# Kernel tuning notes

Measured on AMD Instinct MI355X. Metric: run time of the kernel, lower is better.

Reference implementation:

```python
import math
import jax, jax.numpy as jnp
import numpy as np

N_EMBD = 1024
N_HEAD = 16
HEAD_DIM = N_EMBD // N_HEAD
B, T = 4, 2048
LN_EPS = 1e-5


def setup_inputs() -> dict:
    key = jax.random.key(0)
    ks = jax.random.split(key, 20)
    s = 0.02
    d = {
        'x': jax.random.normal(ks[0], (B, T, N_EMBD), jnp.float32),
        'Wq': jax.random.normal(ks[1], (N_EMBD, N_EMBD), jnp.float32) * s,
        'bq': jnp.zeros((N_EMBD,), jnp.float32),
        'Wk': jax.random.normal(ks[2], (N_EMBD, N_EMBD), jnp.float32) * s,
        'bk': jnp.zeros((N_EMBD,), jnp.float32),
        'Wv': jax.random.normal(ks[3], (N_EMBD, N_EMBD), jnp.float32) * s,
        'bv': jnp.zeros((N_EMBD,), jnp.float32),
        'Wo': jax.random.normal(ks[4], (N_EMBD, N_EMBD), jnp.float32) * s,
        'bo': jnp.zeros((N_EMBD,), jnp.float32),
        'ln1_g': jnp.ones((N_EMBD,), jnp.float32),
        'ln1_b': jnp.zeros((N_EMBD,), jnp.float32),
        'ln2_g': jnp.ones((N_EMBD,), jnp.float32),
        'ln2_b': jnp.zeros((N_EMBD,), jnp.float32),
        'W_fc': jax.random.normal(ks[5], (N_EMBD, 4 * N_EMBD), jnp.float32) * s,
        'b_fc': jnp.zeros((4 * N_EMBD,), jnp.float32),
        'W_proj': jax.random.normal(ks[6], (4 * N_EMBD, N_EMBD), jnp.float32) * s,
        'b_proj': jnp.zeros((N_EMBD,), jnp.float32),
    }
    return d


def _layernorm(x, g, b):
    mu = jnp.mean(x, axis=-1, keepdims=True)
    var = jnp.var(x, axis=-1, keepdims=True)
    return (x - mu) * jax.lax.rsqrt(var + LN_EPS) * g + b


def _new_gelu(x):
    c = math.sqrt(2.0 / math.pi)
    return 0.5 * x * (1.0 + jnp.tanh(c * (x + 0.044715 * x ** 3)))


def _attn(x, Wq, bq, Wk, bk, Wv, bv, Wo, bo):
    Bq, Tq, C = x.shape
    def heads(y):  # (B,T,C) -> (B,H,T,D)
        return y.reshape(Bq, Tq, N_HEAD, HEAD_DIM).transpose(0, 2, 1, 3)
    q = heads(x @ Wq + bq)
    k = heads(x @ Wk + bk)
    v = heads(x @ Wv + bv)
    scores = jnp.einsum('bhqd,bhkd->bhqk', q, k) / math.sqrt(HEAD_DIM)
    causal = jnp.tril(jnp.ones((Tq, Tq), bool))
    scores = jnp.where(causal, scores, -jnp.inf)
    w = jax.nn.softmax(scores, axis=-1)
    av = jnp.einsum('bhqk,bhkd->bhqd', w, v)
    av = av.transpose(0, 2, 1, 3).reshape(Bq, Tq, C)
    return av @ Wo + bo


def reference(x, Wq, bq, Wk, bk, Wv, bv, Wo, bo, ln1_g, ln1_b, ln2_g, ln2_b, W_fc, b_fc, W_proj, b_proj):
    x = x + _attn(_layernorm(x, ln1_g, ln1_b), Wq, bq, Wk, bk, Wv, bv, Wo, bo)
    h = _layernorm(x, ln2_g, ln2_b)
    x = x + (_new_gelu(h @ W_fc + b_fc) @ W_proj + b_proj)
    return x
```

## Files before the change

### kernel.cpp

```cpp
#include <hip/hip_runtime.h>

typedef __attribute__((ext_vector_type(8))) short short8;
typedef __attribute__((ext_vector_type(4))) short short4v;
typedef __attribute__((ext_vector_type(4))) float floatx4;
typedef unsigned short u16;

#define MFMA16(a,b,c) __builtin_amdgcn_mfma_f32_16x16x32_bf16(a,b,c,0,0,0)

typedef const __attribute__((address_space(1))) void* gas1;
typedef __attribute__((address_space(3))) void* las3;
static __device__ __forceinline__ void glds16(const void* g, void* l){
  __builtin_amdgcn_global_load_lds((gas1)g, (las3)l, 16, 0, 0);
}

static __device__ __forceinline__ u16 f2b(float f){
  union { float f; unsigned int u; } c; c.f = f;
  unsigned int u = c.u;
  u += 0x7fffu + ((u >> 16) & 1u);
  return (u16)(u >> 16);
}

__global__ __launch_bounds__(256) void transpose_cvt(
    const float* __restrict__ W, u16* __restrict__ Wt, int K, int N){
  __shared__ float tile[32][33];
  const int tx = threadIdx.x & 31;
  const int ty = threadIdx.x >> 5;
  const int nx = blockIdx.x * 32, kx = blockIdx.y * 32;
  #pragma unroll
  for (int i = ty; i < 32; i += 8)
    tile[i][tx] = W[(size_t)(kx + i) * N + nx + tx];
  __syncthreads();
  #pragma unroll
  for (int i = ty; i < 32; i += 8)
    Wt[(size_t)(nx + i) * K + kx + tx] = f2b(tile[tx][i]);
}

__global__ __launch_bounds__(256) void ln_kernel(
    const float* __restrict__ x, const float* __restrict__ g,
    const float* __restrict__ b, u16* __restrict__ out){
  const int row = blockIdx.x, tid = threadIdx.x;
  const float4 v = reinterpret_cast<const float4*>(x + (size_t)row * 1024)[tid];
  float s  = v.x + v.y + v.z + v.w;
  float s2 = v.x*v.x + v.y*v.y + v.z*v.z + v.w*v.w;
  #pragma unroll
  for (int off = 1; off < 64; off <<= 1){
    s  += __shfl_xor(s,  off);
    s2 += __shfl_xor(s2, off);
  }
  __shared__ float red[8];
  const int wave = tid >> 6, lane = tid & 63;
  if (lane == 0){ red[wave] = s; red[4 + wave] = s2; }
  __syncthreads();
  s  = red[0] + red[1] + red[2] + red[3];
  s2 = red[4] + red[5] + red[6] + red[7];
  const float mu  = s * (1.f/1024.f);
  const float var = s2 * (1.f/1024.f) - mu * mu;
  const float rs  = rsqrtf(var + 1e-5f);
  const float4 gg = reinterpret_cast<const float4*>(g)[tid];
  const float4 bb = reinterpret_cast<const float4*>(b)[tid];
  ushort4 o;
  o.x = f2b((v.x - mu) * rs * gg.x + bb.x);
  o.y = f2b((v.y - mu) * rs * gg.y + bb.y);
  o.z = f2b((v.z - mu) * rs * gg.z + bb.z);
  o.w = f2b((v.w - mu) * rs * gg.w + bb.w);
  reinterpret_cast<ushort4*>(out + (size_t)row * 1024)[tid] = o;
}

__global__ __launch_bounds__(256) void bias_concat(
    const float* __restrict__ bq, const float* __restrict__ bk,
    const float* __restrict__ bv, float* __restrict__ o){
  const int i = blockIdx.x * 256 + threadIdx.x;
  if (i < 1024) o[i] = bq[i];
  else if (i < 2048) o[i] = bk[i - 1024];
  else if (i < 3072) o[i] = bv[i - 2048];
}

template<bool GELU, bool RES, bool OUTBF, bool QKVMODE>
__global__ __launch_bounds__(512) void gemm256(
    const u16* __restrict__ A, const u16* __restrict__ Bt,
    const float* __restrict__ bias,
    const float* __restrict__ res,
    float* __restrict__ outF, u16* __restrict__ outB,
    u16* __restrict__ vtb,
    int M, int N, int K)
{
  __shared__ __attribute__((aligned(16))) u16 sA[2][2][256 * 32];
  __shared__ __attribute__((aligned(16))) u16 sB[2][2][256 * 32];
  const int tid  = threadIdx.x;
  const int wave = tid >> 6, lane = tid & 63, ql = lane >> 4, l16 = lane & 15;
  const int wr = wave >> 2, wc = wave & 3;
  const int m0 = blockIdx.x * 256, n0 = blockIdx.y * 256;

  const int scol = ((lane & 3) ^ ((lane >> 3) & 3)) * 8;
  const u16* aBase = A  + (size_t)(m0 + wave*16 + (lane >> 2)) * K + scol;
  const u16* bBase = Bt + (size_t)(n0 + wr*64 + 4*(lane >> 2) + wc) * K + scol;
  const size_t hK = (size_t)128 * K;
  const int qx = (ql ^ ((l16 >> 1) & 3)) * 8;

  floatx4 acc[8][4];
  #pragma unroll
  for (int i = 0; i < 8; i++)
    #pragma unroll
    for (int nt = 0; nt < 4; nt++) acc[i][nt] = floatx4{0.f,0.f,0.f,0.f};
  short8 af[4], bf[4];

#define STAGE(B_, T_) do { \
    const size_t ko_ = (size_t)(T_) * 64; \
    glds16(aBase + ko_,           &sA[B_][0][wave*512]); \
    glds16(aBase + ko_ + 32,      &sA[B_][1][wave*512]); \
    glds16(aBase + ko_ + hK,      &sA[B_][0][4096 + wave*512]); \
    glds16(aBase + ko_ + hK + 32, &sA[B_][1][4096 + wave*512]); \
    glds16(bBase + ko_,           &sB[B_][0][wave*512]); \
    glds16(bBase + ko_ + 32,      &sB[B_][1][wave*512]); \
    glds16(bBase + ko_ + hK,      &sB[B_][0][4096 + wave*512]); \
    glds16(bBase + ko_ + hK + 32, &sB[B_][1][4096 + wave*512]); \
  } while(0)
#define LDA(B_, KH_, Q_) do { \
    _Pragma("unroll") \
    for (int ii_ = 0; ii_ < 4; ii_++) \
      af[ii_] = *reinterpret_cast<const short8*>( \
          &sA[B_][KH_][(wr*128 + (Q_)*64 + ii_*16 + l16)*32 + qx]); \
  } while(0)
#define LDB(B_, KH_) do { \
    _Pragma("unroll") \
    for (int nt_ = 0; nt_ < 4; nt_++) \
      bf[nt_] = *reinterpret_cast<const short8*>( \
          &sB[B_][KH_][(wc*64 + nt_*16 + l16)*32 + qx]); \
  } while(0)
#define MM(Q_) do { \
    __builtin_amdgcn_s_setprio(1); \
    _Pragma("unroll") \
    for (int ii_ = 0; ii_ < 4; ii_++) \
      _Pragma("unroll") \
      for (int nt_ = 0; nt_ < 4; nt_++) \
        acc[(Q_)*4 + ii_][nt_] = MFMA16(af[ii_], bf[nt_], acc[(Q_)*4 + ii_][nt_]); \
    __builtin_amdgcn_s_setprio(0); \
  } while(0)
#define BAR() do { asm volatile("" ::: "memory"); \
    __builtin_amdgcn_s_barrier(); asm volatile("" ::: "memory"); } while(0)
#define WAITV(N_) asm volatile("s_waitcnt vmcnt(" #N_ ")" ::: "memory")

  const int ntile = K >> 6;
  STAGE(0, 0);

  #pragma unroll 1
  for (int t = 0; t < ntile; t += 2){
    STAGE(1, t + 1);
    WAITV(8);
    BAR();
    LDB(0, 0); LDA(0, 0, 0); MM(0);
    BAR();
    LDA(0, 0, 1); BAR(); MM(1); BAR();
    LDB(0, 1); LDA(0, 1, 0); BAR(); MM(0); BAR();
    LDA(0, 1, 1); BAR(); MM(1); BAR();
    if (t + 2 < ntile){ STAGE(0, t + 2); WAITV(8); }
    else              { WAITV(0); }
    BAR();
    LDB(1, 0); LDA(1, 0, 0); MM(0);
    BAR();
    LDA(1, 0, 1); BAR(); MM(1); BAR();
    LDB(1, 1); LDA(1, 1, 0); BAR(); MM(0); BAR();
    LDA(1, 1, 1); BAR(); MM(1); BAR();
  }

#undef STAGE
#undef LDA
#undef LDB
#undef MM
#undef BAR
#undef WAITV

  const int col0 = n0 + wc*64 + 4*l16;
  const floatx4 bi = *reinterpret_cast<const floatx4*>(&bias[col0]);

  if (QKVMODE && n0 >= 2048){
    #pragma unroll
    for (int nt = 0; nt < 4; nt++){
      const int hd = col0 + nt - 2048;
      u16* vcol = vtb + (size_t)(hd >> 6) * 131072 + (size_t)(hd & 63) * 2048;
      #pragma unroll
      for (int i = 0; i < 8; i++){
        const int t0 = m0 + wr*128 + i*16 + ql*4;
        const int bb = t0 >> 11, tt = t0 & 2047;
        short4v pk;
        #pragma unroll
        for (int r = 0; r < 4; r++) pk[r] = (short)f2b(acc[i][nt][r] + bi[nt]);
        *reinterpret_cast<short4v*>(vcol + (size_t)bb * 2097152 + tt) = pk;
      }
    }
    return;
  }

  #pragma unroll
  for (int i = 0; i < 8; i++){
    #pragma unroll
    for (int r = 0; r < 4; r++){
      const int row = m0 + wr*128 + i*16 + ql*4 + r;
      if (OUTBF){
        short4v o;
        #pragma unroll
        for (int nt = 0; nt < 4; nt++){
          float val = acc[i][nt][r] + bi[nt];
          if (GELU){
            const float t = 0.7978845608028654f * (val + 0.044715f * val * val * val);
            val = val / (1.f + __expf(-2.f * t));
          }
          o[nt] = (short)f2b(val);
        }
        *reinterpret_cast<short4v*>(&outB[(size_t)row * N + col0]) = o;
      } else {
        floatx4 v;
        #pragma unroll
        for (int nt = 0; nt < 4; nt++) v[nt] = acc[i][nt][r] + bi[nt];
        if (RES){
          const floatx4 rr = *reinterpret_cast<const floatx4*>(&res[(size_t)row * N + col0]);
          #pragma unroll
          for (int nt = 0; nt < 4; nt++) v[nt] += rr[nt];
        }
        *reinterpret_cast<floatx4*>(&outF[(size_t)row * N + col0]) = v;
      }
    }
  }
}

__global__ __launch_bounds__(256) void attn_kernel(
    const u16* __restrict__ qkv, const u16* __restrict__ vtb,
    u16* __restrict__ O)
{
  constexpr int T = 2048, LDQ = 3072, LDP = 72;
  __shared__ __attribute__((aligned(16))) u16 sK[2][2][64*32];
  __shared__ __attribute__((aligned(16))) u16 sV[2][2][64*32];
  __shared__ __attribute__((aligned(16))) u16 sP[4][16*LDP];

  const int tid = threadIdx.x, wave = tid >> 6, lane = tid & 63;
  const int quad = lane >> 4, l16 = lane & 15;

  const int lin = blockIdx.y * 16 + blockIdx.x;
  const int j = lin & 15;
  const int bh = lin >> 4;
  const int kk4 = bh >> 4;
  const int jj = (j + ((kk4 & 2) << 2)) & 15;
  const int qt = (kk4 & 1) ? (15 - jj) : jj;
  const int q0 = qt * 128;
  const int b = bh >> 4, h = bh & 15;

  const u16* Qp = qkv + (size_t)b * T * LDQ + h * 64;
  const u16* Kp = Qp + 1024;
  const u16* Vt = vtb + (size_t)bh * 64 * T;

  const int qx = (quad ^ ((l16 >> 1) & 3)) * 8;

  int qg[2]; qg[0] = q0 + wave*16 + l16; qg[1] = qg[0] + 64;
  short8 qf[2][2];
  #pragma unroll
  for (int g = 0; g < 2; g++){
    qf[g][0] = *reinterpret_cast<const short8*>(&Qp[(size_t)qg[g]*LDQ + quad*8]);
    qf[g][1] = *reinterpret_cast<const short8*>(&Qp[(size_t)qg[g]*LDQ + 32 + quad*8]);
  }

  float m_i[2] = {-INFINITY, -INFINITY}, l_i[2] = {0.f, 0.f};
  floatx4 o_acc[2][4];
  #pragma unroll
  for (int g = 0; g < 2; g++)
    #pragma unroll
    for (int nt = 0; nt < 4; nt++) o_acc[g][nt] = floatx4{0.f,0.f,0.f,0.f};

  const int srow = wave*16 + (lane >> 2);
  const int scol = ((lane & 3) ^ ((lane >> 3) & 3)) * 8;
  const int asrc = (lane & 48) | (quad * 4);

  const int kend = q0 + 128;

  {
    glds16(Kp + (size_t)srow*LDQ + scol,      sK[0][0] + wave*512);
    glds16(Kp + (size_t)srow*LDQ + 32 + scol, sK[0][1] + wave*512);
    glds16(Vt + (size_t)srow*T + scol,        sV[0][0] + wave*512);
    glds16(Vt + (size_t)srow*T + 32 + scol,   sV[0][1] + wave*512);
  }

  int buf = 0;
  for (int k0 = 0; k0 < kend; k0 += 64, buf ^= 1){
    __syncthreads();
    if (k0 + 64 < kend){
      const int kn = k0 + 64;
      glds16(Kp + (size_t)(kn + srow)*LDQ + scol,      sK[buf^1][0] + wave*512);
      glds16(Kp + (size_t)(kn + srow)*LDQ + 32 + scol, sK[buf^1][1] + wave*512);
      glds16(Vt + (size_t)srow*T + kn + scol,          sV[buf^1][0] + wave*512);
      glds16(Vt + (size_t)srow*T + kn + 32 + scol,     sV[buf^1][1] + wave*512);
    }

    #pragma unroll
    for (int g = 0; g < 2; g++){
      if (g == 0 && k0 > q0) continue;

      float s[4][4];
      #pragma unroll
      for (int sub = 0; sub < 4; sub++){
        floatx4 sa = floatx4{0.f,0.f,0.f,0.f};
        const short8 kf0 = *reinterpret_cast<const short8*>(&sK[buf][0][(sub*16 + l16)*32 + qx]);
        const short8 kf1 = *reinterpret_cast<const short8*>(&sK[buf][1][(sub*16 + l16)*32 + qx]);
        sa = MFMA16(kf0, qf[g][0], sa);
        sa = MFMA16(kf1, qf[g][1], sa);
        #pragma unroll
        for (int r = 0; r < 4; r++) s[sub][r] = sa[r];
      }
      if (k0 == q0 + g*64){
        #pragma unroll
        for (int sub = 0; sub < 4; sub++)
          #pragma unroll
          for (int r = 0; r < 4; r++){
            const int kidx = k0 + sub*16 + quad*4 + r;
            if (kidx > qg[g]) s[sub][r] = -1e30f;
          }
      }

      float mx = s[0][0];
      #pragma unroll
      for (int sub = 0; sub < 4; sub++)
        #pragma unroll
        for (int r = 0; r < 4; r++) mx = fmaxf(mx, s[sub][r]);
      mx = fmaxf(mx, __shfl_xor(mx, 16));
      mx = fmaxf(mx, __shfl_xor(mx, 32));
      const float mnew  = fmaxf(m_i[g], mx);
      const float alpha = __expf(0.125f * (m_i[g] - mnew));
      float p[4][4], rowsum = 0.f;
      #pragma unroll
      for (int sub = 0; sub < 4; sub++)
        #pragma unroll
        for (int r = 0; r < 4; r++){
          p[sub][r] = __expf(0.125f * (s[sub][r] - mnew));
          rowsum += p[sub][r];
        }
      rowsum += __shfl_xor(rowsum, 16);
      rowsum += __shfl_xor(rowsum, 32);
      l_i[g] = l_i[g] * alpha + rowsum;
      m_i[g] = mnew;

      float arow[4];
      #pragma unroll
      for (int r = 0; r < 4; r++) arow[r] = __shfl(alpha, asrc + r);
      #pragma unroll
      for (int nt = 0; nt < 4; nt++)
        #pragma unroll
        for (int r = 0; r < 4; r++) o_acc[g][nt][r] *= arow[r];

      #pragma unroll
      for (int sub = 0; sub < 4; sub++){
        short4v pk;
        pk[0] = (short)f2b(p[sub][0]); pk[1] = (short)f2b(p[sub][1]);
        pk[2] = (short)f2b(p[sub][2]); pk[3] = (short)f2b(p[sub][3]);
        *reinterpret_cast<short4v*>(&sP[wave][l16*LDP + sub*16 + quad*4]) = pk;
      }
      const short8 pf0 = *reinterpret_cast<const short8*>(&sP[wave][l16*LDP + quad*8]);
      const short8 pf1 = *reinterpret_cast<const short8*>(&sP[wave][l16*LDP + 32 + quad*8]);
      #pragma unroll
      for (int nt = 0; nt < 4; nt++){
        const short8 vf0 = *reinterpret_cast<const short8*>(&sV[buf][0][(nt*16 + l16)*32 + qx]);
        const short8 vf1 = *reinterpret_cast<const short8*>(&sV[buf][1][(nt*16 + l16)*32 + qx]);
        o_acc[g][nt] = MFMA16(pf0, vf0, o_acc[g][nt]);
        o_acc[g][nt] = MFMA16(pf1, vf1, o_acc[g][nt]);
      }
    }
  }

  #pragma unroll
  for (int g = 0; g < 2; g++){
    float lrow[4];
    #pragma unroll
    for (int r = 0; r < 4; r++) lrow[r] = __shfl(l_i[g], asrc + r);
    #pragma unroll
    for (int nt = 0; nt < 4; nt++){
      #pragma unroll
      for (int r = 0; r < 4; r++){
        const int row = q0 + g*64 + wave*16 + quad*4 + r;
        O[(size_t)(b*T + row)*1024 + h*64 + nt*16 + l16] = f2b(o_acc[g][nt][r] / lrow[r]);
      }
    }
  }
}

extern "C" void kernel_launch(void* const* d_in, const int* in_sizes, int n_in,
                              void* d_out, int out_size, void* d_ws, size_t ws_size,
                              hipStream_t stream){
  const float* x      = (const float*)d_in[0];
  const float* Wq     = (const float*)d_in[1];
  const float* bq     = (const float*)d_in[2];
  const float* Wk     = (const float*)d_in[3];
  const float* bk     = (const float*)d_in[4];
  const float* Wv     = (const float*)d_in[5];
  const float* bv     = (const float*)d_in[6];
  const float* Wo     = (const float*)d_in[7];
  const float* bo     = (const float*)d_in[8];
  const float* ln1_g  = (const float*)d_in[9];
  const float* ln1_b  = (const float*)d_in[10];
  const float* ln2_g  = (const float*)d_in[11];
  const float* ln2_b  = (const float*)d_in[12];
  const float* W_fc   = (const float*)d_in[13];
  const float* b_fc   = (const float*)d_in[14];
  const float* W_proj = (const float*)d_in[15];
  const float* b_proj = (const float*)d_in[16];
  float* out = (float*)d_out;
  char* ws = (char*)d_ws;
  const size_t MB = 1024 * 1024;

  u16* bufA  = (u16*)(ws);
  u16* qkvb  = (u16*)(ws + 16*MB);
  u16* vtb   = (u16*)(ws + 64*MB);
  u16* fcb   = (u16*)(ws + 16*MB);
  float* x2  = out;
  u16* Wqkvt = (u16*)(ws + 80*MB);
  u16* Wot   = (u16*)(ws + 86*MB);
  u16* Wfct  = (u16*)(ws + 88*MB);
  u16* Wpjt  = (u16*)(ws + 96*MB);
  float* bqkv= (float*)(ws + 104*MB);

  dim3 tb(256), tg(512);
  transpose_cvt<<<dim3(32, 32),  tb, 0, stream>>>(Wq,     Wqkvt,             1024, 1024);
  transpose_cvt<<<dim3(32, 32),  tb, 0, stream>>>(Wk,     Wqkvt + 1024*1024, 1024, 1024);
  transpose_cvt<<<dim3(32, 32),  tb, 0, stream>>>(Wv,     Wqkvt + 2048*1024, 1024, 1024);
  transpose_cvt<<<dim3(32, 32),  tb, 0, stream>>>(Wo,     Wot,               1024, 1024);
  transpose_cvt<<<dim3(128, 32), tb, 0, stream>>>(W_fc,   Wfct,              1024, 4096);
  transpose_cvt<<<dim3(32, 128), tb, 0, stream>>>(W_proj, Wpjt,              4096, 1024);
  bias_concat<<<dim3(12), tb, 0, stream>>>(bq, bk, bv, bqkv);

  ln_kernel<<<8192, tb, 0, stream>>>(x, ln1_g, ln1_b, bufA);

  gemm256<false,false,true,true><<<dim3(32,12), tg, 0, stream>>>(
      bufA, Wqkvt, bqkv, nullptr, nullptr, qkvb, vtb, 8192, 3072, 1024);

  attn_kernel<<<dim3(16, 64), tb, 0, stream>>>(qkvb, vtb, bufA);

  gemm256<false,true,false,false><<<dim3(32,4), tg, 0, stream>>>(
      bufA, Wot, bo, x, x2, nullptr, nullptr, 8192, 1024, 1024);

  ln_kernel<<<8192, tb, 0, stream>>>(x2, ln2_g, ln2_b, bufA);

  gemm256<true,false,true,false><<<dim3(32,16), tg, 0, stream>>>(
      bufA, Wfct, b_fc, nullptr, nullptr, fcb, nullptr, 8192, 4096, 1024);

  gemm256<false,true,false,false><<<dim3(32,4), tg, 0, stream>>>(
      fcb, Wpjt, b_proj, x2, out, nullptr, nullptr, 8192, 1024, 4096);
}
```

Measured before the change: 616.3 us.

## Interleave global-to-LDS prefetch in quarters between MFMA phases of GEMM mainloop

Splits each K-tile's global-to-LDS stage into four partial loads (A and B halves by K-subtile) and spreads them across the eight MFMA phases of the double-buffered loop, with finer vmcnt waits. The aim is to overlap memory traffic with compute more evenly instead of issuing all eight loads in a burst at the start of each half-iteration. Wait counts and barriers are rearranged, which risks exposing latency if the partial waits are too tight or leaving a race if ordering is wrong.

```diff
diff --git a/kernel.cpp b/kernel.cpp
--- a/kernel.cpp
+++ b/kernel.cpp
@@ -104,16 +104,15 @@
     for (int nt = 0; nt < 4; nt++) acc[i][nt] = floatx4{0.f,0.f,0.f,0.f};
   short8 af[4], bf[4];
 
-#define STAGE(B_, T_) do { \
-    const size_t ko_ = (size_t)(T_) * 64; \
-    glds16(aBase + ko_,           &sA[B_][0][wave*512]); \
-    glds16(aBase + ko_ + 32,      &sA[B_][1][wave*512]); \
-    glds16(aBase + ko_ + hK,      &sA[B_][0][4096 + wave*512]); \
-    glds16(aBase + ko_ + hK + 32, &sA[B_][1][4096 + wave*512]); \
-    glds16(bBase + ko_,           &sB[B_][0][wave*512]); \
-    glds16(bBase + ko_ + 32,      &sB[B_][1][wave*512]); \
-    glds16(bBase + ko_ + hK,      &sB[B_][0][4096 + wave*512]); \
-    glds16(bBase + ko_ + hK + 32, &sB[B_][1][4096 + wave*512]); \
+#define STG2(B_, T_, P_) do { \
+    const size_t ko_ = (size_t)(T_) * 64 + (((P_) >> 1) ? 32 : 0); \
+    if ((P_) & 1){ \
+      glds16(bBase + ko_,      &sB[B_][(P_)>>1][wave*512]); \
+      glds16(bBase + ko_ + hK, &sB[B_][(P_)>>1][4096 + wave*512]); \
+    } else { \
+      glds16(aBase + ko_,      &sA[B_][(P_)>>1][wave*512]); \
+      glds16(aBase + ko_ + hK, &sA[B_][(P_)>>1][4096 + wave*512]); \
+    } \
   } while(0)
 #define LDA(B_, KH_, Q_) do { \
     _Pragma("unroll") \
@@ -141,29 +140,34 @@
 #define WAITV(N_) asm volatile("s_waitcnt vmcnt(" #N_ ")" ::: "memory")
 
   const int ntile = K >> 6;
-  STAGE(0, 0);
+  STG2(0, 0, 0); STG2(0, 0, 1); STG2(0, 0, 2); STG2(0, 0, 3);
+  WAITV(4);
+  BAR();
 
   #pragma unroll 1
   for (int t = 0; t < ntile; t += 2){
-    STAGE(1, t + 1);
-    WAITV(8);
-    BAR();
-    LDB(0, 0); LDA(0, 0, 0); MM(0);
-    BAR();
-    LDA(0, 0, 1); BAR(); MM(1); BAR();
-    LDB(0, 1); LDA(0, 1, 0); BAR(); MM(0); BAR();
-    LDA(0, 1, 1); BAR(); MM(1); BAR();
-    if (t + 2 < ntile){ STAGE(0, t + 2); WAITV(8); }
-    else              { WAITV(0); }
-    BAR();
-    LDB(1, 0); LDA(1, 0, 0); MM(0);
-    BAR();
-    LDA(1, 0, 1); BAR(); MM(1); BAR();
-    LDB(1, 1); LDA(1, 1, 0); BAR(); MM(0); BAR();
-    LDA(1, 1, 1); BAR(); MM(1); BAR();
-  }
-
-#undef STAGE
+    const bool more = (t + 2 < ntile);
+    LDB(0,0); LDA(0,0,0); STG2(1, t+1, 0);
+    BAR(); MM(0); BAR();
+    LDA(0,0,1); STG2(1, t+1, 1); WAITV(4);
+    BAR(); MM(1); BAR();
+    LDB(0,1); LDA(0,1,0); STG2(1, t+1, 2);
+    BAR(); MM(0); BAR();
+    LDA(0,1,1); STG2(1, t+1, 3); WAITV(4);
+    BAR(); MM(1); BAR();
+    LDB(1,0); LDA(1,0,0); if (more) STG2(0, t+2, 0);
+    BAR(); MM(0); BAR();
+    LDA(1,0,1);
+    if (more){ STG2(0, t+2, 1); WAITV(4); } else { WAITV(0); }
+    BAR(); MM(1); BAR();
+    LDB(1,1); LDA(1,1,0); if (more) STG2(0, t+2, 2);
+    BAR(); MM(0); BAR();
+    LDA(1,1,1);
+    if (more){ STG2(0, t+2, 3); WAITV(4); }
+    BAR(); MM(1); BAR();
+  }
+
+#undef STG2
 #undef LDA
 #undef LDB
 #undef MM
```

Result: faster. 592.1 us (-3.9%).
